# Kernel tuning notes

Hardware: AMD Instinct MI355X
Metric: run time of the kernel (lower is better)

The kernel has to match this reference:

```python
import jax, jax.numpy as jnp
import numpy as np

B, T, C = 4, 2048, 1024
NH = 16
HD = C // NH  # 64


def setup_inputs() -> dict:
    key = jax.random.key(0)
    k1, k2, k3, k4, k5 = jax.random.split(key, 5)
    s_in = 1.0 / np.sqrt(C)
    return {
        "x": jax.random.normal(k1, (B, T, C), dtype=jnp.float32),
        "attention_mask": jnp.ones((B, T), dtype=jnp.float32),
        "W_qkv": jax.random.normal(k2, (C, 3 * C), dtype=jnp.float32) * s_in,
        "b_qkv": jnp.zeros((3 * C,), dtype=jnp.float32),
        "W_out": jax.random.normal(k3, (C, C), dtype=jnp.float32) * s_in,
        "b_out": jnp.zeros((C,), dtype=jnp.float32),
    }


def reference(x, attention_mask, W_qkv, b_qkv, W_out, b_out):
    Bx, Tx, Cx = x.shape
    # QKV projection: (B,T,3C)
    qkv = x @ W_qkv + b_qkv
    Q, K, V = jnp.split(qkv, 3, axis=-1)
    # (B, NH, T, HD)
    Q = Q.reshape(Bx, Tx, NH, HD).transpose(0, 2, 1, 3)
    K = K.reshape(Bx, Tx, NH, HD).transpose(0, 2, 1, 3)
    V = V.reshape(Bx, Tx, NH, HD).transpose(0, 2, 1, 3)
    # scaled scores (B, NH, T, T)
    scores = jnp.einsum("bhqd,bhkd->bhqk", Q, K) * (1.0 / np.sqrt(HD))
    # causal mask: set strictly-upper triangle to -inf (mask-fill semantics)
    causal = jnp.tril(jnp.ones((Tx, Tx), dtype=bool))[None, None]
    scores = jnp.where(causal, scores, -jnp.inf)
    # additive padding mask
    pad = (1.0 - attention_mask)[:, None, None, :] * jnp.finfo(scores.dtype).min
    scores = scores + pad
    attn = jax.nn.softmax(scores, axis=-1)
    # weighted values -> (B, T, C)
    wv = jnp.einsum("bhqk,bhkd->bhqd", attn, V)
    wv = wv.transpose(0, 2, 1, 3).reshape(Bx, Tx, Cx)
    return wv @ W_out + b_out
```

## Files before the change

kernel.cpp:

```cpp
#include <hip/hip_runtime.h>
#include <math.h>

constexpr int BB = 4;
constexpr int TT = 2048;
constexpr int CC = 1024;
constexpr int NHH = 16;
constexpr int HDD = 64;
constexpr int C3 = 3 * CC;

typedef __bf16 bf16x8 __attribute__((ext_vector_type(8)));
typedef float  f32x4  __attribute__((ext_vector_type(4)));

__device__ __forceinline__ unsigned short f2bf(float x) {
    union { float f; unsigned u; } v; v.f = x;
    unsigned r = v.u + 0x7fffu + ((v.u >> 16) & 1u);
    return (unsigned short)(r >> 16);
}

#define AS1(p) ((const __attribute__((address_space(1))) void*)(p))
#define AS3(p) ((__attribute__((address_space(3))) void*)(p))

constexpr float SM2 = 17.312340490667561f;

constexpr int CAST_BLOCKS = (BB * TT * CC / 4) / 256;
constexpr int TQKV_BLOCKS = (C3 / 64) * (CC / 64);
constexpr int TOUT_BLOCKS = (CC / 64) * (CC / 64);
constexpr int KB_BLOCKS   = (BB * TT) / 256;

__global__ __launch_bounds__(256) void prep(
    const float* __restrict__ x,
    const float* __restrict__ Wqkv,
    const float* __restrict__ Wout,
    const float* __restrict__ amask,
    unsigned short* __restrict__ xb,
    unsigned short* __restrict__ Wqkvt,
    unsigned short* __restrict__ Woutt,
    float* __restrict__ kbias)
{
    __shared__ float tile[64][65];
    const int bid = blockIdx.x;
    const int t = threadIdx.x;

    if (bid < CAST_BLOCKS) {
        const int i = bid * 256 + t;
        float4 v = ((const float4*)x)[i];
        ushort4 o;
        o.x = f2bf(v.x); o.y = f2bf(v.y); o.z = f2bf(v.z); o.w = f2bf(v.w);
        ((ushort4*)xb)[i] = o;
        return;
    }
    if (bid >= CAST_BLOCKS + TQKV_BLOCKS + TOUT_BLOCKS) {
        const int i = (bid - CAST_BLOCKS - TQKV_BLOCKS - TOUT_BLOCKS) * 256 + t;
        kbias[i] = (amask[i] - 1.0f) * 1.0e38f - SM2;
        return;
    }

    const float* src; unsigned short* dst; int R, Cn, r0, c0;
    if (bid < CAST_BLOCKS + TQKV_BLOCKS) {
        const int tb = bid - CAST_BLOCKS;
        src = Wqkv; dst = Wqkvt; R = CC; Cn = C3;
        c0 = (tb % (C3 / 64)) * 64; r0 = (tb / (C3 / 64)) * 64;
    } else {
        const int tb = bid - CAST_BLOCKS - TQKV_BLOCKS;
        src = Wout; dst = Woutt; R = CC; Cn = CC;
        c0 = (tb % (CC / 64)) * 64; r0 = (tb / (CC / 64)) * 64;
    }

    const int lr = t >> 4, lc = (t & 15) * 4;
    #pragma unroll
    for (int s = 0; s < 4; ++s) {
        float4 v = *(const float4*)&src[(size_t)(r0 + lr + s * 16) * Cn + c0 + lc];
        tile[lr + s * 16][lc + 0] = v.x;
        tile[lr + s * 16][lc + 1] = v.y;
        tile[lr + s * 16][lc + 2] = v.z;
        tile[lr + s * 16][lc + 3] = v.w;
    }
    __syncthreads();
    const int oi = t >> 2, oc = (t & 3) * 16;
    unsigned short buf[16];
    #pragma unroll
    for (int u = 0; u < 16; ++u)
        buf[u] = f2bf(tile[oc + u][oi]);
    unsigned short* d = &dst[(size_t)(c0 + oi) * R + r0 + oc];
    *(uint4*)(d + 0) = *(uint4*)&buf[0];
    *(uint4*)(d + 8) = *(uint4*)&buf[8];
}

template<bool VSPLIT>
__global__ __launch_bounds__(256) void gemm_bt_mfma(
    const unsigned short* __restrict__ A,
    const unsigned short* __restrict__ Bt,
    const float* __restrict__ bias,
    float* __restrict__ OutF,
    unsigned short* __restrict__ Qp,
    unsigned short* __restrict__ Kp,
    unsigned short* __restrict__ Vtp,
    int M, int N, int K, float qscale)
{
    __shared__ alignas(16) unsigned short As[128 * 64];
    __shared__ alignas(16) unsigned short Bs[128 * 64];

    const int tid  = threadIdx.x;
    const int w    = tid >> 6;
    const int lane = tid & 63;
    const int quad = lane >> 4;
    const int col  = lane & 15;
    const int m0 = blockIdx.y * 128, n0 = blockIdx.x * 128;
    const int wr = w >> 1, wc = w & 1;

    f32x4 acc[4][4];
    #pragma unroll
    for (int i = 0; i < 4; ++i)
        #pragma unroll
        for (int j = 0; j < 4; ++j)
            #pragma unroll
            for (int r = 0; r < 4; ++r)
                acc[i][j][r] = 0.0f;

    const int srow = tid >> 3;
    const int spos = tid & 7;
    char* AsB = (char*)As;
    char* BsB = (char*)Bs;

    for (int k0 = 0; k0 < K; k0 += 64) {
        if (k0) __syncthreads();
        #pragma unroll
        for (int i = 0; i < 4; ++i) {
            const int row = srow + 32 * i;
            const int sch = spos ^ (row & 7);
            __builtin_amdgcn_global_load_lds(
                AS1(A + (size_t)(m0 + row) * K + k0 + sch * 8),
                AS3(AsB + i * 4096 + w * 1024), 16, 0, 0);
            __builtin_amdgcn_global_load_lds(
                AS1(Bt + (size_t)(n0 + row) * K + k0 + sch * 8),
                AS3(BsB + i * 4096 + w * 1024), 16, 0, 0);
        }
        __syncthreads();

        #pragma unroll
        for (int ks = 0; ks < 2; ++ks) {
            bf16x8 af[4], bf[4];
            #pragma unroll
            for (int i = 0; i < 4; ++i) {
                const int ra = wr * 64 + i * 16 + col;
                const int pa = ((quad + ks * 4) ^ (ra & 7)) * 8;
                af[i] = *(const bf16x8*)&As[ra * 64 + pa];
                const int rb = wc * 64 + i * 16 + col;
                const int pb = ((quad + ks * 4) ^ (rb & 7)) * 8;
                bf[i] = *(const bf16x8*)&Bs[rb * 64 + pb];
            }
            #pragma unroll
            for (int i = 0; i < 4; ++i)
                #pragma unroll
                for (int j = 0; j < 4; ++j)
                    acc[i][j] = __builtin_amdgcn_mfma_f32_16x16x32_bf16(af[i], bf[j], acc[i][j], 0, 0, 0);
        }
    }

    if (VSPLIT) {
        if (n0 < CC) {
            #pragma unroll
            for (int i = 0; i < 4; ++i)
                #pragma unroll
                for (int r = 0; r < 4; ++r) {
                    const int m = m0 + wr * 64 + i * 16 + quad * 4 + r;
                    #pragma unroll
                    for (int j = 0; j < 4; ++j) {
                        const int n = n0 + wc * 64 + j * 16 + col;
                        Qp[(size_t)m * CC + n] = f2bf((acc[i][j][r] + bias[n]) * qscale);
                    }
                }
        } else if (n0 < 2 * CC) {
            #pragma unroll
            for (int i = 0; i < 4; ++i) {
                const int mb   = m0 + wr * 64 + i * 16 + quad * 4;
                const int bidx = mb >> 11;
                const int tloc = mb & 2047;
                #pragma unroll
                for (int j = 0; j < 4; ++j) {
                    const int n  = n0 + wc * 64 + j * 16 + col;
                    const int hh = (n - CC) >> 6;
                    const int dd = (n - CC) & 63;
                    #pragma unroll
                    for (int r = 0; r < 4; ++r)
                        Kp[(((size_t)bidx * NHH + hh) * TT + tloc + r) * HDD + dd] =
                            f2bf(acc[i][j][r] + bias[n]);
                }
            }
        } else {
            #pragma unroll
            for (int i = 0; i < 4; ++i) {
                const int mb   = m0 + wr * 64 + i * 16 + quad * 4;
                const int bidx = mb >> 11;
                const int tloc = mb & 2047;
                const int ktile = tloc >> 6, tc = tloc & 63;
                #pragma unroll
                for (int j = 0; j < 4; ++j) {
                    const int n  = n0 + wc * 64 + j * 16 + col;
                    const int hh = (n - 2 * CC) >> 6;
                    const int dd = (n - 2 * CC) & 63;
                    unsigned short pk[4];
                    #pragma unroll
                    for (int r = 0; r < 4; ++r)
                        pk[r] = f2bf(acc[i][j][r] + bias[n]);
                    *(uint2*)&Vtp[((((size_t)bidx * NHH + hh) * 32 + ktile) * HDD + dd) * 64 + tc] =
                        *(const uint2*)pk;
                }
            }
        }
    } else {
        #pragma unroll
        for (int i = 0; i < 4; ++i)
            #pragma unroll
            for (int r = 0; r < 4; ++r) {
                const int m = m0 + wr * 64 + i * 16 + quad * 4 + r;
                #pragma unroll
                for (int j = 0; j < 4; ++j) {
                    const int n = n0 + wc * 64 + j * 16 + col;
                    OutF[(size_t)m * N + n] = acc[i][j][r] + bias[n];
                }
            }
    }
}

constexpr int PP = 72;

__global__ __launch_bounds__(512, 6) void attn_mfma(
    const unsigned short* __restrict__ Qp,
    const unsigned short* __restrict__ Kp,
    const unsigned short* __restrict__ Vtp,
    const float* __restrict__ kbias,
    unsigned short* __restrict__ WV)
{
    __shared__ alignas(16) unsigned short Ks [2][64 * 64];
    __shared__ alignas(16) unsigned short Vts[2][64 * 64];
    __shared__ alignas(16) __bf16        Ps[8][16 * PP];

    const int tid  = threadIdx.x;
    const int w    = tid >> 6;
    const int lane = tid & 63;
    const int quad = lane >> 4;
    const int col  = lane & 15;
    const int bh = blockIdx.y, b = bh >> 4, h = bh & 15;
    const int jx = blockIdx.x;

    const unsigned short* Qg = Qp + (size_t)b * TT * CC + (size_t)h * HDD;
    const unsigned short* Kg = Kp + (size_t)bh * TT * HDD;
    const unsigned short* Vg = Vtp + (size_t)bh * 32 * HDD * 64;
    const float* kb_g = kbias + b * TT;

    const int srow = tid >> 3;
    const int sch  = (tid & 7) ^ (srow & 7);
    char* KsB  = (char*)&Ks[0][0];
    char* VtsB = (char*)&Vts[0][0];

    #pragma unroll
    for (int ph = 0; ph < 2; ++ph) {
        const int qb    = ph ? (15 - jx) : jx;
        const int qbase = qb * 128;
        const int qw    = qbase + w * 16;

        bf16x8 qf0 = *(const bf16x8*)(Qg + (size_t)(qw + col) * CC + quad * 8);
        bf16x8 qf1 = *(const bf16x8*)(Qg + (size_t)(qw + col) * CC + 32 + quad * 8);

        f32x4 o[4];
        float l[4];
        #pragma unroll
        for (int t = 0; t < 4; ++t)
            #pragma unroll
            for (int r = 0; r < 4; ++r) o[t][r] = 0.0f;
        #pragma unroll
        for (int r = 0; r < 4; ++r) l[r] = 0.0f;

        const int ntiles = 2 * qb + 2;

        __builtin_amdgcn_global_load_lds(
            AS1(Kg + (size_t)srow * HDD + sch * 8), AS3(KsB + w * 1024), 16, 0, 0);
        __builtin_amdgcn_global_load_lds(
            AS1(Vg + (size_t)srow * 64 + sch * 8), AS3(VtsB + w * 1024), 16, 0, 0);
        __syncthreads();

        for (int it = 0; it < ntiles; ++it) {
            const int kt  = it << 6;
            const int cur = it & 1;

            if (it + 1 < ntiles) {
                __builtin_amdgcn_global_load_lds(
                    AS1(Kg + (size_t)(kt + 64 + srow) * HDD + sch * 8),
                    AS3(KsB + (cur ^ 1) * 8192 + w * 1024), 16, 0, 0);
                __builtin_amdgcn_global_load_lds(
                    AS1(Vg + ((size_t)(it + 1) * 64 + srow) * 64 + sch * 8),
                    AS3(VtsB + (cur ^ 1) * 8192 + w * 1024), 16, 0, 0);
            }

            if (kt <= qw + 15) {
                const unsigned short* ksb = &Ks[cur][0];
                const unsigned short* vsb = &Vts[cur][0];

                float kb[4];
                #pragma unroll
                for (int t = 0; t < 4; ++t)
                    kb[t] = kb_g[kt + t * 16 + col];

                f32x4 s[4];
                #pragma unroll
                for (int t = 0; t < 4; ++t) {
                    const int row = t * 16 + col;
                    const int c0 = (quad ^ (row & 7)) * 8;
                    const int c1 = ((quad + 4) ^ (row & 7)) * 8;
                    bf16x8 k0 = *(const bf16x8*)&ksb[row * 64 + c0];
                    bf16x8 k1 = *(const bf16x8*)&ksb[row * 64 + c1];
                    f32x4 z;
                    #pragma unroll
                    for (int r = 0; r < 4; ++r) z[r] = kb[t];
                    z = __builtin_amdgcn_mfma_f32_16x16x32_bf16(qf0, k0, z, 0, 0, 0);
                    z = __builtin_amdgcn_mfma_f32_16x16x32_bf16(qf1, k1, z, 0, 0, 0);
                    s[t] = z;
                }

                const bool needc = (kt + 64 > qw);
                #pragma unroll
                for (int t = 0; t < 4; ++t) {
                    const int key = kt + t * 16 + col;
                    #pragma unroll
                    for (int r = 0; r < 4; ++r) {
                        float p = __builtin_amdgcn_exp2f(s[t][r]);
                        if (needc && key > qw + quad * 4 + r) p = 0.0f;
                        l[r] += p;
                        Ps[w][(quad * 4 + r) * PP + t * 16 + col] = (__bf16)p;
                    }
                }

                bf16x8 p0 = *(const bf16x8*)&Ps[w][col * PP + quad * 8];
                bf16x8 p1 = *(const bf16x8*)&Ps[w][col * PP + 32 + quad * 8];
                #pragma unroll
                for (int t = 0; t < 4; ++t) {
                    const int row = t * 16 + col;
                    const int c0 = (quad ^ (row & 7)) * 8;
                    const int c1 = ((quad + 4) ^ (row & 7)) * 8;
                    bf16x8 v0 = *(const bf16x8*)&vsb[row * 64 + c0];
                    bf16x8 v1 = *(const bf16x8*)&vsb[row * 64 + c1];
                    o[t] = __builtin_amdgcn_mfma_f32_16x16x32_bf16(p0, v0, o[t], 0, 0, 0);
                    o[t] = __builtin_amdgcn_mfma_f32_16x16x32_bf16(p1, v1, o[t], 0, 0, 0);
                }
            }
            __syncthreads();
        }

        #pragma unroll
        for (int off = 1; off < 16; off <<= 1)
            #pragma unroll
            for (int r = 0; r < 4; ++r)
                l[r] += __shfl_xor(l[r], off);
        #pragma unroll
        for (int r = 0; r < 4; ++r) {
            const float inv = 1.0f / l[r];
            const int q = qw + quad * 4 + r;
            unsigned short* dst = WV + ((size_t)b * TT + q) * CC + (size_t)h * HDD;
            #pragma unroll
            for (int t = 0; t < 4; ++t)
                dst[t * 16 + col] = f2bf(o[t][r] * inv);
        }
    }
}

extern "C" void kernel_launch(void* const* d_in, const int* in_sizes, int n_in,
                              void* d_out, int out_size, void* d_ws, size_t ws_size,
                              hipStream_t stream) {
    const float* x     = (const float*)d_in[0];
    const float* amask = (const float*)d_in[1];
    const float* Wqkv  = (const float*)d_in[2];
    const float* bqkv  = (const float*)d_in[3];
    const float* Wout  = (const float*)d_in[4];
    const float* bout  = (const float*)d_in[5];
    float* out = (float*)d_out;

    const int M = BB * TT;

    unsigned short* xb    = (unsigned short*)d_ws;
    unsigned short* Wqkvt = xb    + (size_t)M * CC;
    unsigned short* Woutt = Wqkvt + (size_t)C3 * CC;
    unsigned short* Qp    = Woutt + (size_t)CC * CC;
    unsigned short* Kp    = Qp    + (size_t)M * CC;
    unsigned short* Vtp   = Kp    + (size_t)M * CC;
    unsigned short* wvb   = Vtp   + (size_t)M * CC;
    float*          kbias = (float*)(wvb + (size_t)M * CC);

    dim3 blk(256);

    prep<<<dim3(CAST_BLOCKS + TQKV_BLOCKS + TOUT_BLOCKS + KB_BLOCKS), blk, 0, stream>>>(
        x, Wqkv, Wout, amask, xb, Wqkvt, Woutt, kbias);

    gemm_bt_mfma<true><<<dim3(C3 / 128, M / 128), blk, 0, stream>>>(
        xb, Wqkvt, bqkv, nullptr, Qp, Kp, Vtp, M, C3, CC, 0.18033688011112043f);
    attn_mfma<<<dim3(TT / 256, BB * NHH), dim3(512), 0, stream>>>(
        Qp, Kp, Vtp, kbias, wvb);
    gemm_bt_mfma<false><<<dim3(CC / 128, M / 128), blk, 0, stream>>>(
        wvb, Woutt, bout, out, nullptr, nullptr, nullptr, M, CC, CC, 1.0f);
}
```

Baseline: 258.2 us.

## Give each attention wave 32 query rows and remap blocks across XCDs

The attention kernel now runs 4 waves of 256 threads per block instead of 8, and each wave handles two 16-row query sub-tiles. Each K/V fragment read from LDS therefore feeds twice as many MFMAs, and the block loads the K/V tile in two passes per thread. The 1D grid is remapped so that consecutive block IDs, which round-robin across the XCDs, place all blocks of one batch-head on the same XCD for L2 reuse. The cost is more registers per wave and half as many waves per block for hiding latency, and the causal skip check is now per 32 rows, so some masked work is wasted.

```diff
diff --git a/kernel.cpp b/kernel.cpp
--- a/kernel.cpp
+++ b/kernel.cpp
@@ -225,7 +225,7 @@
 
 constexpr int PP = 72;
 
-__global__ __launch_bounds__(512, 6) void attn_mfma(
+__global__ __launch_bounds__(256, 2) void attn_mfma(
     const unsigned short* __restrict__ Qp,
     const unsigned short* __restrict__ Kp,
     const unsigned short* __restrict__ Vtp,
@@ -234,15 +234,17 @@
 {
     __shared__ alignas(16) unsigned short Ks [2][64 * 64];
     __shared__ alignas(16) unsigned short Vts[2][64 * 64];
-    __shared__ alignas(16) __bf16        Ps[8][16 * PP];
+    __shared__ alignas(16) __bf16        Ps[4][32 * PP];
 
     const int tid  = threadIdx.x;
     const int w    = tid >> 6;
     const int lane = tid & 63;
     const int quad = lane >> 4;
     const int col  = lane & 15;
-    const int bh = blockIdx.y, b = bh >> 4, h = bh & 15;
-    const int jx = blockIdx.x;
+
+    const int wid = ((blockIdx.x & 7) << 6) | (blockIdx.x >> 3);
+    const int bh = wid >> 3, jx = wid & 7;
+    const int b = bh >> 4, h = bh & 15;
 
     const unsigned short* Qg = Qp + (size_t)b * TT * CC + (size_t)h * HDD;
     const unsigned short* Kg = Kp + (size_t)bh * TT * HDD;
@@ -258,26 +260,37 @@
     for (int ph = 0; ph < 2; ++ph) {
         const int qb    = ph ? (15 - jx) : jx;
         const int qbase = qb * 128;
-        const int qw    = qbase + w * 16;
-
-        bf16x8 qf0 = *(const bf16x8*)(Qg + (size_t)(qw + col) * CC + quad * 8);
-        bf16x8 qf1 = *(const bf16x8*)(Qg + (size_t)(qw + col) * CC + 32 + quad * 8);
-
-        f32x4 o[4];
-        float l[4];
-        #pragma unroll
-        for (int t = 0; t < 4; ++t)
-            #pragma unroll
-            for (int r = 0; r < 4; ++r) o[t][r] = 0.0f;
-        #pragma unroll
-        for (int r = 0; r < 4; ++r) l[r] = 0.0f;
+        const int qw    = qbase + w * 32;
+
+        bf16x8 qfa0 = *(const bf16x8*)(Qg + (size_t)(qw + col) * CC + quad * 8);
+        bf16x8 qfa1 = *(const bf16x8*)(Qg + (size_t)(qw + col) * CC + 32 + quad * 8);
+        bf16x8 qfb0 = *(const bf16x8*)(Qg + (size_t)(qw + 16 + col) * CC + quad * 8);
+        bf16x8 qfb1 = *(const bf16x8*)(Qg + (size_t)(qw + 16 + col) * CC + 32 + quad * 8);
+
+        f32x4 o[2][4];
+        float l[2][4];
+        #pragma unroll
+        for (int hh = 0; hh < 2; ++hh)
+            #pragma unroll
+            for (int t = 0; t < 4; ++t)
+                #pragma unroll
+                for (int r = 0; r < 4; ++r) o[hh][t][r] = 0.0f;
+        #pragma unroll
+        for (int hh = 0; hh < 2; ++hh)
+            #pragma unroll
+            for (int r = 0; r < 4; ++r) l[hh][r] = 0.0f;
 
         const int ntiles = 2 * qb + 2;
 
-        __builtin_amdgcn_global_load_lds(
-            AS1(Kg + (size_t)srow * HDD + sch * 8), AS3(KsB + w * 1024), 16, 0, 0);
-        __builtin_amdgcn_global_load_lds(
-            AS1(Vg + (size_t)srow * 64 + sch * 8), AS3(VtsB + w * 1024), 16, 0, 0);
+        #pragma unroll
+        for (int i = 0; i < 2; ++i) {
+            __builtin_amdgcn_global_load_lds(
+                AS1(Kg + (size_t)(srow + 32 * i) * HDD + sch * 8),
+                AS3(KsB + i * 4096 + w * 1024), 16, 0, 0);
+            __builtin_amdgcn_global_load_lds(
+                AS1(Vg + (size_t)(srow + 32 * i) * 64 + sch * 8),
+                AS3(VtsB + i * 4096 + w * 1024), 16, 0, 0);
+        }
         __syncthreads();
 
         for (int it = 0; it < ntiles; ++it) {
@@ -285,15 +298,18 @@
             const int cur = it & 1;
 
             if (it + 1 < ntiles) {
-                __builtin_amdgcn_global_load_lds(
-                    AS1(Kg + (size_t)(kt + 64 + srow) * HDD + sch * 8),
-                    AS3(KsB + (cur ^ 1) * 8192 + w * 1024), 16, 0, 0);
-                __builtin_amdgcn_global_load_lds(
-                    AS1(Vg + ((size_t)(it + 1) * 64 + srow) * 64 + sch * 8),
-                    AS3(VtsB + (cur ^ 1) * 8192 + w * 1024), 16, 0, 0);
-            }
-
-            if (kt <= qw + 15) {
+                #pragma unroll
+                for (int i = 0; i < 2; ++i) {
+                    __builtin_amdgcn_global_load_lds(
+                        AS1(Kg + (size_t)(kt + 64 + srow + 32 * i) * HDD + sch * 8),
+                        AS3(KsB + (cur ^ 1) * 8192 + i * 4096 + w * 1024), 16, 0, 0);
+                    __builtin_amdgcn_global_load_lds(
+                        AS1(Vg + ((size_t)(it + 1) * 64 + srow + 32 * i) * 64 + sch * 8),
+                        AS3(VtsB + (cur ^ 1) * 8192 + i * 4096 + w * 1024), 16, 0, 0);
+                }
+            }
+
+            if (kt <= qw + 31) {
                 const unsigned short* ksb = &Ks[cur][0];
                 const unsigned short* vsb = &Vts[cur][0];
 
@@ -302,7 +318,7 @@
                 for (int t = 0; t < 4; ++t)
                     kb[t] = kb_g[kt + t * 16 + col];
 
-                f32x4 s[4];
+                f32x4 s[2][4];
                 #pragma unroll
                 for (int t = 0; t < 4; ++t) {
                     const int row = t * 16 + col;
@@ -313,26 +329,33 @@
                     f32x4 z;
                     #pragma unroll
                     for (int r = 0; r < 4; ++r) z[r] = kb[t];
-                    z = __builtin_amdgcn_mfma_f32_16x16x32_bf16(qf0, k0, z, 0, 0, 0);
-                    z = __builtin_amdgcn_mfma_f32_16x16x32_bf16(qf1, k1, z, 0, 0, 0);
-                    s[t] = z;
+                    f32x4 za = __builtin_amdgcn_mfma_f32_16x16x32_bf16(qfa0, k0, z, 0, 0, 0);
+                    za = __builtin_amdgcn_mfma_f32_16x16x32_bf16(qfa1, k1, za, 0, 0, 0);
+                    s[0][t] = za;
+                    f32x4 zb = __builtin_amdgcn_mfma_f32_16x16x32_bf16(qfb0, k0, z, 0, 0, 0);
+                    zb = __builtin_amdgcn_mfma_f32_16x16x32_bf16(qfb1, k1, zb, 0, 0, 0);
+                    s[1][t] = zb;
                 }
 
                 const bool needc = (kt + 64 > qw);
                 #pragma unroll
-                for (int t = 0; t < 4; ++t) {
-                    const int key = kt + t * 16 + col;
+                for (int hh = 0; hh < 2; ++hh)
                     #pragma unroll
-                    for (int r = 0; r < 4; ++r) {
-                        float p = __builtin_amdgcn_exp2f(s[t][r]);
-                        if (needc && key > qw + quad * 4 + r) p = 0.0f;
-                        l[r] += p;
-                        Ps[w][(quad * 4 + r) * PP + t * 16 + col] = (__bf16)p;
+                    for (int t = 0; t < 4; ++t) {
+                        const int key = kt + t * 16 + col;
+                        #pragma unroll
+                        for (int r = 0; r < 4; ++r) {
+                            float p = __builtin_amdgcn_exp2f(s[hh][t][r]);
+                            if (needc && key > qw + hh * 16 + quad * 4 + r) p = 0.0f;
+                            l[hh][r] += p;
+                            Ps[w][(hh * 16 + quad * 4 + r) * PP + t * 16 + col] = (__bf16)p;
+                        }
                     }
-                }
-
-                bf16x8 p0 = *(const bf16x8*)&Ps[w][col * PP + quad * 8];
-                bf16x8 p1 = *(const bf16x8*)&Ps[w][col * PP + 32 + quad * 8];
+
+                bf16x8 p0a = *(const bf16x8*)&Ps[w][col * PP + quad * 8];
+                bf16x8 p1a = *(const bf16x8*)&Ps[w][col * PP + 32 + quad * 8];
+                bf16x8 p0b = *(const bf16x8*)&Ps[w][(16 + col) * PP + quad * 8];
+                bf16x8 p1b = *(const bf16x8*)&Ps[w][(16 + col) * PP + 32 + quad * 8];
                 #pragma unroll
                 for (int t = 0; t < 4; ++t) {
                     const int row = t * 16 + col;
@@ -340,26 +363,31 @@
                     const int c1 = ((quad + 4) ^ (row & 7)) * 8;
                     bf16x8 v0 = *(const bf16x8*)&vsb[row * 64 + c0];
                     bf16x8 v1 = *(const bf16x8*)&vsb[row * 64 + c1];
-                    o[t] = __builtin_amdgcn_mfma_f32_16x16x32_bf16(p0, v0, o[t], 0, 0, 0);
-                    o[t] = __builtin_amdgcn_mfma_f32_16x16x32_bf16(p1, v1, o[t], 0, 0, 0);
+                    o[0][t] = __builtin_amdgcn_mfma_f32_16x16x32_bf16(p0a, v0, o[0][t], 0, 0, 0);
+                    o[0][t] = __builtin_amdgcn_mfma_f32_16x16x32_bf16(p1a, v1, o[0][t], 0, 0, 0);
+                    o[1][t] = __builtin_amdgcn_mfma_f32_16x16x32_bf16(p0b, v0, o[1][t], 0, 0, 0);
+                    o[1][t] = __builtin_amdgcn_mfma_f32_16x16x32_bf16(p1b, v1, o[1][t], 0, 0, 0);
                 }
             }
             __syncthreads();
         }
 
         #pragma unroll
-        for (int off = 1; off < 16; off <<= 1)
-            #pragma unroll
-            for (int r = 0; r < 4; ++r)
-                l[r] += __shfl_xor(l[r], off);
-        #pragma unroll
-        for (int r = 0; r < 4; ++r) {
-            const float inv = 1.0f / l[r];
-            const int q = qw + quad * 4 + r;
-            unsigned short* dst = WV + ((size_t)b * TT + q) * CC + (size_t)h * HDD;
-            #pragma unroll
-            for (int t = 0; t < 4; ++t)
-                dst[t * 16 + col] = f2bf(o[t][r] * inv);
+        for (int hh = 0; hh < 2; ++hh) {
+            #pragma unroll
+            for (int off = 1; off < 16; off <<= 1)
+                #pragma unroll
+                for (int r = 0; r < 4; ++r)
+                    l[hh][r] += __shfl_xor(l[hh][r], off);
+            #pragma unroll
+            for (int r = 0; r < 4; ++r) {
+                const float inv = 1.0f / l[hh][r];
+                const int q = qw + hh * 16 + quad * 4 + r;
+                unsigned short* dst = WV + ((size_t)b * TT + q) * CC + (size_t)h * HDD;
+                #pragma unroll
+                for (int t = 0; t < 4; ++t)
+                    dst[t * 16 + col] = f2bf(o[hh][t][r] * inv);
+            }
         }
     }
 }
@@ -393,7 +421,7 @@
 
     gemm_bt_mfma<true><<<dim3(C3 / 128, M / 128), blk, 0, stream>>>(
         xb, Wqkvt, bqkv, nullptr, Qp, Kp, Vtp, M, C3, CC, 0.18033688011112043f);
-    attn_mfma<<<dim3(TT / 256, BB * NHH), dim3(512), 0, stream>>>(
+    attn_mfma<<<dim3(512), dim3(256), 0, stream>>>(
         Qp, Kp, Vtp, kbias, wvb);
     gemm_bt_mfma<false><<<dim3(CC / 128, M / 128), blk, 0, stream>>>(
         wvb, Woutt, bout, out, nullptr, nullptr, nullptr, M, CC, CC, 1.0f);
```

New measurement: 257.2 us. About the same (-0.4%).
